# Optimization experiments

Hardware: AMD Instinct MI355X
Metric: run time of the kernel (lower is better)

The kernel has to match this reference:

```python
import jax, jax.numpy as jnp
import numpy as np

N = 8192
IN_F = 512
OUT_F = 64
NEG_SLOPE = 0.01  # nn.LeakyReLU default
MASK_VAL = -1e9


def setup_inputs() -> dict:
    key = jax.random.key(0)
    k_h, k_adj, k_W, k_a = jax.random.split(key, 4)
    h = jax.random.normal(k_h, (N, IN_F), dtype=jnp.float32)
    adjacency = jax.random.randint(k_adj, (N, N), 0, 2, dtype=jnp.int32)
    # xavier_uniform bounds
    bW = float(np.sqrt(6.0 / (IN_F + OUT_F)))
    ba = float(np.sqrt(6.0 / (2 * OUT_F + 1)))
    W = jax.random.uniform(k_W, (IN_F, OUT_F), minval=-bW, maxval=bW, dtype=jnp.float32)
    a = jax.random.uniform(k_a, (2 * OUT_F, 1), minval=-ba, maxval=ba, dtype=jnp.float32)
    return {"h": h, "adjacency": adjacency, "W": W, "a": a}


def reference(h, adjacency, W, a):
    WH = h @ W                                  # [N, out_f]
    wh1 = WH @ a[:OUT_F, :]                     # [N, 1]
    wh2 = WH @ a[OUT_F:, :]                     # [N, 1]
    e = jax.nn.leaky_relu(wh1 + wh2.T, negative_slope=NEG_SLOPE)  # [N, N]
    attnt = jnp.where(adjacency > 0, e, jnp.float32(MASK_VAL))
    attnt = jax.nn.softmax(attnt, axis=1)       # row-wise softmax
    hfirst = attnt @ WH                         # [N, out_f]
    return jax.nn.elu(hfirst)
```

## Files before the change

kernel.cpp:

```cpp
#include <hip/hip_runtime.h>
#include <hip/hip_bf16.h>

#define N 8192
#define IN_F 512
#define OUT_F 64
#define S_SPLIT 16
#define JT (N / S_SPLIT)
#define NB (N / 8)
#define WHB 128
#define PACKB ((N / 32) * (N / 256) * 4)
#define LOG2E 1.44269504088896340736f

typedef __attribute__((ext_vector_type(8))) short short8;
typedef __attribute__((ext_vector_type(4))) float floatx4;
typedef __attribute__((ext_vector_type(4))) int intx4;

__device__ inline short f2bf(float x) {
    __hip_bfloat16 b = __float2bfloat16(x);
    return __builtin_bit_cast(short, b);
}

__device__ inline float fexp2(float x) {
#if __has_builtin(__builtin_amdgcn_exp2f)
    return __builtin_amdgcn_exp2f(x);
#else
    return exp2f(x);
#endif
}

__global__ void k_wt(const float* __restrict__ W, short* __restrict__ WT) {
    int idx = blockIdx.x * 256 + threadIdx.x;
    int k = idx >> 6, f = idx & 63;
    WT[f * IN_F + k] = f2bf(W[k * OUT_F + f]);
}

__global__ __launch_bounds__(256) void k_packwh(const int* __restrict__ adj,
                                                unsigned* __restrict__ mask,
                                                const float* __restrict__ h,
                                                const short* __restrict__ WT,
                                                const float* __restrict__ a,
                                                short* __restrict__ WHbT,
                                                float* __restrict__ wh1,
                                                float* __restrict__ wh2) {
    __shared__ float tileS[4][OUT_F][17];
    int tid = threadIdx.x;

    if (blockIdx.x >= WHB) {
        int bid = blockIdx.x - WHB;
        int wv = (bid * 256 + tid) >> 6;
        int lane = tid & 63;
        const int* p = adj + (size_t)wv * 512 + lane;
        unsigned long long m0 = __ballot(p[0]   > 0);
        unsigned long long m1 = __ballot(p[64]  > 0);
        unsigned long long m2 = __ballot(p[128] > 0);
        unsigned long long m3 = __ballot(p[192] > 0);
        unsigned long long m4 = __ballot(p[256] > 0);
        unsigned long long m5 = __ballot(p[320] > 0);
        unsigned long long m6 = __ballot(p[384] > 0);
        unsigned long long m7 = __ballot(p[448] > 0);
        if (lane < 16) {
            unsigned long long s0 = (lane & 2) ? m1 : m0;
            unsigned long long s1 = (lane & 2) ? m3 : m2;
            unsigned long long s2 = (lane & 2) ? m5 : m4;
            unsigned long long s3 = (lane & 2) ? m7 : m6;
            unsigned long long t0 = (lane & 4) ? s1 : s0;
            unsigned long long t1 = (lane & 4) ? s3 : s2;
            unsigned long long u  = (lane & 8) ? t1 : t0;
            unsigned dw = (lane & 1) ? (unsigned)(u >> 32) : (unsigned)u;
            mask[wv * 16 + lane] = dw;
        }
        return;
    }

    int w = tid >> 6, lane = tid & 63;
    int n = lane & 15, q = lane >> 4;
    int i0 = (blockIdx.x * 4 + w) * 16;
    float (*tile)[17] = tileS[w];
    const float* hp = h + (size_t)(i0 + n) * IN_F + q * 8;
    floatx4 acc[4] = {};
#pragma unroll
    for (int k0 = 0; k0 < IN_F; k0 += 32) {
        floatx4 h0 = *(const floatx4*)(hp + k0);
        floatx4 h1 = *(const floatx4*)(hp + k0 + 4);
        short8 af;
#pragma unroll
        for (int j = 0; j < 4; j++) { af[j] = f2bf(h0[j]); af[j + 4] = f2bf(h1[j]); }
#pragma unroll
        for (int b = 0; b < 4; b++) {
            short8 bf_ = *(const short8*)(WT + (b * 16 + n) * IN_F + k0 + q * 8);
            acc[b] = __builtin_amdgcn_mfma_f32_16x16x32_bf16(af, bf_, acc[b], 0, 0, 0);
        }
    }
#pragma unroll
    for (int b = 0; b < 4; b++)
#pragma unroll
        for (int r = 0; r < 4; r++)
            tile[b * 16 + n][q * 4 + r] = acc[b][r];
    float a1v[4], a2v[4];
#pragma unroll
    for (int b = 0; b < 4; b++) { a1v[b] = a[b * 16 + n]; a2v[b] = a[OUT_F + b * 16 + n]; }
#pragma unroll
    for (int r = 0; r < 4; r++) {
        float s1 = 0.f, s2 = 0.f;
#pragma unroll
        for (int b = 0; b < 4; b++) { s1 += acc[b][r] * a1v[b]; s2 += acc[b][r] * a2v[b]; }
#pragma unroll
        for (int m = 1; m <= 8; m <<= 1) {
            s1 += __shfl_xor(s1, m, 64);
            s2 += __shfl_xor(s2, m, 64);
        }
        if (n == 0) {
            wh1[i0 + q * 4 + r] = s1 * LOG2E;
            wh2[i0 + q * 4 + r] = s2 * LOG2E;
        }
    }
    __syncthreads();
    const float* tc = tile[lane & 63];
    short8 s0, s1v;
#pragma unroll
    for (int k = 0; k < 8; k++) { s0[k] = f2bf(tc[k]); s1v[k] = f2bf(tc[k + 8]); }
    *(short8*)(WHbT + (size_t)lane * N + i0) = s0;
    *(short8*)(WHbT + (size_t)lane * N + i0 + 8) = s1v;
}

__global__ __launch_bounds__(256, 3) void k_attn(const unsigned char* __restrict__ mask,
                                                 const short* __restrict__ WHbT,
                                                 const float* __restrict__ wh1,
                                                 const float* __restrict__ wh2,
                                                 float* __restrict__ num_part,
                                                 float* __restrict__ den_part) {
    int tid = threadIdx.x;
    int w = tid >> 6;
    int lane = tid & 63;
    int n = lane & 15, q = lane >> 4;
    int split = blockIdx.y;
    int j0 = split * JT;
    int i0 = blockIdx.x * 256 + w * 64;

    const short* bbase = WHbT + j0 + q * 8;
    short8 b0[4], b1[4];
    auto bload = [&](short8* bb, int s) {
        const short* bp = bbase + s * 32;
#pragma unroll
        for (int b = 0; b < 4; b++)
            bb[b] = *(const short8*)(bp + (size_t)(b * 16 + n) * N);
    };
    bload(b0, 0);

    float wh1f[4];
#pragma unroll
    for (int rf = 0; rf < 4; rf++) wh1f[rf] = wh1[i0 + rf * 16 + n];

    floatx4 acc[4][4] = {};
    floatx4 accd[4] = {};
    const float* w2p = wh2 + j0 + q * 8;

    short8 onesf = {};
    if (n == 0) {
        short o = f2bf(1.0f);
#pragma unroll
        for (int jj = 0; jj < 8; jj++) onesf[jj] = o;
    }

#pragma unroll
    for (int g = 0; g < 4; g++) {
        intx4 mc[4];
#pragma unroll
        for (int rf = 0; rf < 4; rf++)
            mc[rf] = *(const intx4*)(mask + (size_t)(i0 + rf * 16 + n) * NB
                                     + split * 64 + g * 16);
#pragma unroll
        for (int d = 0; d < 4; d++) {
            int s = g * 4 + d;
            if (s < 15) bload((s & 1) ? b0 : b1, s + 1);
            const short8* bb = (s & 1) ? b1 : b0;
            floatx4 w20 = *(const floatx4*)(w2p + s * 32);
            floatx4 w21 = *(const floatx4*)(w2p + s * 32 + 4);
#pragma unroll
            for (int rf = 0; rf < 4; rf++) {
                unsigned md = (unsigned)mc[rf][d] >> (q * 8);
                float p[8];
#pragma unroll
                for (int jj = 0; jj < 8; jj++) {
                    float e = wh1f[rf] + ((jj < 4) ? w20[jj] : w21[jj - 4]);
                    float el = fmaxf(e, 0.01f * e);
                    el = ((md >> jj) & 1u) ? el : -1024.0f;
                    p[jj] = fexp2(el);
                }
                short8 af;
#pragma unroll
                for (int jj = 0; jj < 8; jj++) af[jj] = f2bf(p[jj]);
#pragma unroll
                for (int b = 0; b < 4; b++)
                    acc[rf][b] = __builtin_amdgcn_mfma_f32_16x16x32_bf16(af, bb[b], acc[rf][b], 0, 0, 0);
                accd[rf] = __builtin_amdgcn_mfma_f32_16x16x32_bf16(af, onesf, accd[rf], 0, 0, 0);
            }
        }
    }

#pragma unroll
    for (int rf = 0; rf < 4; rf++)
        if (n == 0)
            *(floatx4*)(den_part + (size_t)split * N + i0 + rf * 16 + q * 4) = accd[rf];

    float* np_ = num_part + (size_t)split * N * OUT_F;
#pragma unroll
    for (int rf = 0; rf < 4; rf++)
#pragma unroll
        for (int b = 0; b < 4; b++)
#pragma unroll
            for (int r = 0; r < 4; r++)
                np_[(size_t)(i0 + rf * 16 + q * 4 + r) * OUT_F + b * 16 + n] = acc[rf][b][r];
}

__global__ void k_final(const float* __restrict__ num_part,
                        const float* __restrict__ den_part,
                        float* __restrict__ out) {
    int t = blockIdx.x * 256 + threadIdx.x;
    int idx4 = t * 4;
    int row = idx4 >> 6;
    floatx4 s = {};
    float d = 0.f;
#pragma unroll
    for (int sp = 0; sp < S_SPLIT; sp++) {
        floatx4 v = *(const floatx4*)(num_part + (size_t)sp * N * OUT_F + idx4);
        s += v;
        d += den_part[sp * N + row];
    }
    floatx4 o;
#pragma unroll
    for (int j = 0; j < 4; j++) {
        float x = s[j] / d;
        o[j] = (x > 0.f) ? x : (__expf(x) - 1.f);
    }
    *(floatx4*)(out + idx4) = o;
}

extern "C" void kernel_launch(void* const* d_in, const int* in_sizes, int n_in,
                              void* d_out, int out_size, void* d_ws, size_t ws_size,
                              hipStream_t stream) {
    const float* h = (const float*)d_in[0];
    const int* adj = (const int*)d_in[1];
    const float* W = (const float*)d_in[2];
    const float* a = (const float*)d_in[3];
    float* out = (float*)d_out;

    char* ws = (char*)d_ws;
    short* WHbT     = (short*)(ws);
    short* WT       = (short*)(ws + (size_t)(1 << 20));
    float* wh1      = (float*)(ws + (size_t)(1 << 20) + (64 << 10));
    float* wh2      = wh1 + N;
    unsigned* maskb = (unsigned*)(ws + (size_t)(2 << 20));
    float* num_p    = (float*)(ws + (size_t)(16 << 20));
    float* den_p    = (float*)(ws + (size_t)(48 << 20));

    k_wt<<<dim3(128), dim3(256), 0, stream>>>(W, WT);
    k_packwh<<<dim3(WHB + PACKB), dim3(256), 0, stream>>>(adj, maskb, h, WT, a,
                                                          WHbT, wh1, wh2);
    k_attn<<<dim3(N / 256, S_SPLIT), dim3(256), 0, stream>>>((const unsigned char*)maskb,
                                                             WHbT, wh1, wh2, num_p, den_p);
    k_final<<<dim3((N * OUT_F) / 1024), dim3(256), 0, stream>>>(num_p, den_p, out);
}
```

Measured before the change: 420.2 us.

## Stage transposed WH tile in shared memory shared across block waves

Before, each of the four waves loaded its own WH B-fragments from global memory, double-buffered in registers. Now the block cooperatively copies a 64x256 bf16 slice of WHbT into padded LDS in two halves, and every wave reads its B-fragments from LDS. This cuts redundant global/L2 traffic by 4x but adds block barriers and drops the register prefetch overlap, so loads and compute can no longer overlap within a wave. LDS use (~33KB) may reduce occupancy under the 3-blocks launch bound.

```diff
diff --git a/kernel.cpp b/kernel.cpp
--- a/kernel.cpp
+++ b/kernel.cpp
@@ -7,6 +7,7 @@
 #define S_SPLIT 16
 #define JT (N / S_SPLIT)
 #define NB (N / 8)
+#define LDW 264
 #define WHB 128
 #define PACKB ((N / 32) * (N / 256) * 4)
 #define LOG2E 1.44269504088896340736f
@@ -129,6 +130,7 @@
                                                  const float* __restrict__ wh2,
                                                  float* __restrict__ num_part,
                                                  float* __restrict__ den_part) {
+    __shared__ short ldsb[OUT_F * LDW];
     int tid = threadIdx.x;
     int w = tid >> 6;
     int lane = tid & 63;
@@ -137,23 +139,13 @@
     int j0 = split * JT;
     int i0 = blockIdx.x * 256 + w * 64;
 
-    const short* bbase = WHbT + j0 + q * 8;
-    short8 b0[4], b1[4];
-    auto bload = [&](short8* bb, int s) {
-        const short* bp = bbase + s * 32;
-#pragma unroll
-        for (int b = 0; b < 4; b++)
-            bb[b] = *(const short8*)(bp + (size_t)(b * 16 + n) * N);
-    };
-    bload(b0, 0);
-
     float wh1f[4];
 #pragma unroll
     for (int rf = 0; rf < 4; rf++) wh1f[rf] = wh1[i0 + rf * 16 + n];
 
     floatx4 acc[4][4] = {};
     floatx4 accd[4] = {};
-    const float* w2p = wh2 + j0 + q * 8;
+    const short* lp = ldsb + q * 8;
 
     short8 onesf = {};
     if (n == 0) {
@@ -162,38 +154,53 @@
         for (int jj = 0; jj < 8; jj++) onesf[jj] = o;
     }
 
-#pragma unroll
-    for (int g = 0; g < 4; g++) {
-        intx4 mc[4];
-#pragma unroll
-        for (int rf = 0; rf < 4; rf++)
-            mc[rf] = *(const intx4*)(mask + (size_t)(i0 + rf * 16 + n) * NB
-                                     + split * 64 + g * 16);
-#pragma unroll
-        for (int d = 0; d < 4; d++) {
-            int s = g * 4 + d;
-            if (s < 15) bload((s & 1) ? b0 : b1, s + 1);
-            const short8* bb = (s & 1) ? b1 : b0;
-            floatx4 w20 = *(const floatx4*)(w2p + s * 32);
-            floatx4 w21 = *(const floatx4*)(w2p + s * 32 + 4);
-#pragma unroll
-            for (int rf = 0; rf < 4; rf++) {
-                unsigned md = (unsigned)mc[rf][d] >> (q * 8);
-                float p[8];
-#pragma unroll
-                for (int jj = 0; jj < 8; jj++) {
-                    float e = wh1f[rf] + ((jj < 4) ? w20[jj] : w21[jj - 4]);
-                    float el = fmaxf(e, 0.01f * e);
-                    el = ((md >> jj) & 1u) ? el : -1024.0f;
-                    p[jj] = fexp2(el);
+    for (int hh = 0; hh < 2; hh++) {
+        __syncthreads();
+#pragma unroll
+        for (int l = 0; l < 8; l++) {
+            int idx = l * 256 + tid;
+            int f = idx >> 5, c = idx & 31;
+            *(short8*)(ldsb + f * LDW + c * 8) =
+                *(const short8*)(WHbT + (size_t)f * N + j0 + hh * 256 + c * 8);
+        }
+        __syncthreads();
+
+        const float* w2p = wh2 + j0 + hh * 256 + q * 8;
+#pragma unroll
+        for (int g = 0; g < 2; g++) {
+            intx4 mc[4];
+#pragma unroll
+            for (int rf = 0; rf < 4; rf++)
+                mc[rf] = *(const intx4*)(mask + (size_t)(i0 + rf * 16 + n) * NB
+                                         + split * 64 + hh * 32 + g * 16);
+#pragma unroll
+            for (int d = 0; d < 4; d++) {
+                int s = g * 4 + d;
+                floatx4 w20 = *(const floatx4*)(w2p + s * 32);
+                floatx4 w21 = *(const floatx4*)(w2p + s * 32 + 4);
+                short8 bfr[4];
+#pragma unroll
+                for (int b = 0; b < 4; b++)
+                    bfr[b] = *(const short8*)(lp + (b * 16 + n) * LDW + s * 32);
+#pragma unroll
+                for (int rf = 0; rf < 4; rf++) {
+                    unsigned md = (unsigned)mc[rf][d] >> (q * 8);
+                    float p[8];
+#pragma unroll
+                    for (int jj = 0; jj < 8; jj++) {
+                        float e = wh1f[rf] + ((jj < 4) ? w20[jj] : w21[jj - 4]);
+                        float el = fmaxf(e, 0.01f * e);
+                        el = ((md >> jj) & 1u) ? el : -1024.0f;
+                        p[jj] = fexp2(el);
+                    }
+                    short8 af;
+#pragma unroll
+                    for (int jj = 0; jj < 8; jj++) af[jj] = f2bf(p[jj]);
+#pragma unroll
+                    for (int b = 0; b < 4; b++)
+                        acc[rf][b] = __builtin_amdgcn_mfma_f32_16x16x32_bf16(af, bfr[b], acc[rf][b], 0, 0, 0);
+                    accd[rf] = __builtin_amdgcn_mfma_f32_16x16x32_bf16(af, onesf, accd[rf], 0, 0, 0);
                 }
-                short8 af;
-#pragma unroll
-                for (int jj = 0; jj < 8; jj++) af[jj] = f2bf(p[jj]);
-#pragma unroll
-                for (int b = 0; b < 4; b++)
-                    acc[rf][b] = __builtin_amdgcn_mfma_f32_16x16x32_bf16(af, bb[b], acc[rf][b], 0, 0, 0);
-                accd[rf] = __builtin_amdgcn_mfma_f32_16x16x32_bf16(af, onesf, accd[rf], 0, 0, 0);
             }
         }
     }
```

After: 416.9 us. About the same (-0.8%).
